# Kernel tuning notes

Measured on AMD Instinct MI355X. Metric: run time of the kernel, lower is better.

## Reference

```python
import jax, jax.numpy as jnp
import numpy as np

N_EMBD = 1024
N_HEAD = 16
HEAD = N_EMBD // N_HEAD  # 64
N_HIDDEN = 2816          # ((int(2*4*1024/3)-1)//256)*256 + 256
BLOCK_SIZE = 4096
EPS = 1e-5


def rope_cos_sin(T, hd, base=10000.0):
    theta = 1.0 / (base ** (jnp.arange(0, hd, 2, dtype=jnp.float32) / hd))  # (hd/2,)
    idx = jnp.arange(T, dtype=jnp.float32)
    ang = jnp.outer(idx, theta)  # (T, hd/2)
    return jnp.cos(ang), jnp.sin(ang)


def apply_rope(x, cos, sin):
    # x: (B, H, T, hd); rotate interleaved pairs (x0,x1),(x2,x3),...
    xp = x.reshape(*x.shape[:-1], HEAD // 2, 2)
    xe, xo = xp[..., 0], xp[..., 1]
    c = cos[None, None, :, :]
    s = sin[None, None, :, :]
    oe = xe * c - xo * s
    oo = xe * s + xo * c
    return jnp.stack([oe, oo], axis=-1).reshape(x.shape)


def rmsnorm(x, scale):
    ms = jnp.mean(x * x, axis=-1, keepdims=True)
    return scale * (x * jax.lax.rsqrt(ms + EPS))


def setup_inputs() -> dict:
    key = jax.random.key(0)
    ks = jax.random.split(key, 9)
    B, T = 2, 2048
    x = jax.random.normal(ks[0], (B, T, N_EMBD), dtype=jnp.float32)
    y_mask = jax.random.randint(ks[1], (B, 64), 0, 2, dtype=jnp.int32)
    sd = 1.0 / np.sqrt(N_EMBD)
    Wqkv = jax.random.normal(ks[2], (N_EMBD, 3 * N_EMBD), dtype=jnp.float32) * sd
    Wattn_proj = jax.random.normal(ks[3], (N_EMBD, N_EMBD), dtype=jnp.float32) * sd
    scale1 = jnp.ones((N_EMBD,), dtype=jnp.float32)
    scale2 = jnp.ones((N_EMBD,), dtype=jnp.float32)
    Wfc1 = jax.random.normal(ks[4], (N_EMBD, N_HIDDEN), dtype=jnp.float32) * sd
    Wfc2 = jax.random.normal(ks[5], (N_EMBD, N_HIDDEN), dtype=jnp.float32) * sd
    Wmlp_proj = jax.random.normal(ks[6], (N_HIDDEN, N_EMBD), dtype=jnp.float32) / np.sqrt(N_HIDDEN)
    return {"x": x, "y_mask": y_mask, "Wqkv": Wqkv, "Wattn_proj": Wattn_proj,
            "scale1": scale1, "scale2": scale2, "Wfc1": Wfc1, "Wfc2": Wfc2,
            "Wmlp_proj": Wmlp_proj}


def reference(x, y_mask, Wqkv, Wattn_proj, scale1, scale2, Wfc1, Wfc2, Wmlp_proj):
    B, T, C = x.shape
    # ---- attention branch (pre-RMSNorm) ----
    h = rmsnorm(x, scale1)
    qkv = h @ Wqkv  # (B, T, 3C)
    q, k, v = jnp.split(qkv, 3, axis=-1)
    q = q.reshape(B, T, N_HEAD, HEAD).transpose(0, 2, 1, 3)
    k = k.reshape(B, T, N_HEAD, HEAD).transpose(0, 2, 1, 3)
    v = v.reshape(B, T, N_HEAD, HEAD).transpose(0, 2, 1, 3)
    cos, sin = rope_cos_sin(T, HEAD)
    q = apply_rope(q, cos, sin)
    k = apply_rope(k, cos, sin)
    # mixed causal + text-text bidirectional mask
    causal = jnp.tril(jnp.ones((T, T), dtype=bool))  # (T, T)
    ym = y_mask.astype(bool)  # (B, L)
    L = ym.shape[1]
    text = ym[:, :, None] & ym[:, None, :]  # (B, L, L)
    text = jnp.pad(text, ((0, 0), (0, T - L), (0, T - L)))
    mask = jnp.logical_or(causal[None, :, :], text)  # (B, T, T)
    scale = 1.0 / np.sqrt(HEAD)
    scores = jnp.einsum('bhqd,bhkd->bhqk', q, k) * scale
    scores = jnp.where(mask[:, None, :, :], scores, -jnp.inf)
    attn = jax.nn.softmax(scores, axis=-1)
    y = jnp.einsum('bhqk,bhkd->bhqd', attn, v)
    y = y.transpose(0, 2, 1, 3).reshape(B, T, C)
    x = x + y @ Wattn_proj
    # ---- SwiGLU MLP branch (pre-RMSNorm) ----
    h2 = rmsnorm(x, scale2)
    m = jax.nn.silu(h2 @ Wfc1) * (h2 @ Wfc2)
    x = x + m @ Wmlp_proj
    return x
```

## Files before the change

### kernel.cpp

```cpp
#include <hip/hip_runtime.h>
#include <stdint.h>

typedef unsigned short u16;
typedef __attribute__((ext_vector_type(8))) short bf16x8;
typedef __attribute__((ext_vector_type(4))) float f32x4;

__device__ __forceinline__ float b2f(u16 u) {
    union { float f; uint32_t u; } v; v.u = ((uint32_t)u) << 16; return v.f;
}
__device__ __forceinline__ u16 f2b(float f) {
    union { float f; uint32_t u; } v; v.f = f;
    uint32_t r = v.u + 0x7FFFu + ((v.u >> 16) & 1u);
    return (u16)(r >> 16);
}

template <int CTRL>
__device__ __forceinline__ float dppf(float x) {
    union { float f; int i; } u; u.f = x;
    u.i = __builtin_amdgcn_update_dpp(0, u.i, CTRL, 0xF, 0xF, false);
    return u.f;
}
__device__ __forceinline__ float rowmax16(float v) {
    v = fmaxf(v, dppf<0x121>(v));
    v = fmaxf(v, dppf<0x122>(v));
    v = fmaxf(v, dppf<0x124>(v));
    v = fmaxf(v, dppf<0x128>(v));
    return v;
}
__device__ __forceinline__ float rowsum16(float v) {
    v += dppf<0x121>(v);
    v += dppf<0x122>(v);
    v += dppf<0x124>(v);
    v += dppf<0x128>(v);
    return v;
}

__device__ __forceinline__ void stage16(const void* g, void* l) {
    __builtin_amdgcn_global_load_lds(
        (const __attribute__((address_space(1))) uint32_t*)(uintptr_t)g,
        (__attribute__((address_space(3))) uint32_t*)(uint32_t)(uintptr_t)l,
        16, 0, 0);
}

__global__ __launch_bounds__(256) void transpose_all(const float* __restrict__ Wqkv,
                                                     const float* __restrict__ Wattn,
                                                     const float* __restrict__ Wfc1,
                                                     const float* __restrict__ Wfc2,
                                                     const float* __restrict__ Wmlp,
                                                     u16* WtQ, u16* WtA, u16* WtF1,
                                                     u16* WtF2, u16* WtM) {
    __shared__ u16 tile[32][33];
    int id = blockIdx.x;
    const float* src; u16* dst; int R, C;
    if (id < 3072)      {             src = Wqkv;  dst = WtQ;  R = 1024; C = 3072; }
    else if (id < 4096) { id -= 3072; src = Wattn; dst = WtA;  R = 1024; C = 1024; }
    else if (id < 6912) { id -= 4096; src = Wfc1;  dst = WtF1; R = 1024; C = 2816; }
    else if (id < 9728) { id -= 6912; src = Wfc2;  dst = WtF2; R = 1024; C = 2816; }
    else                { id -= 9728; src = Wmlp;  dst = WtM;  R = 2816; C = 1024; }
    const int nbx = C >> 5;
    const int bx = id % nbx, by = id / nbx;
    const int cx = bx * 32, ry = by * 32;
    const int tx = threadIdx.x, ty = threadIdx.y;
    #pragma unroll
    for (int i = 0; i < 32; i += 8)
        tile[ty + i][tx] = f2b(src[(size_t)(ry + ty + i) * C + cx + tx]);
    __syncthreads();
    #pragma unroll
    for (int i = 0; i < 32; i += 8)
        dst[(size_t)(cx + ty + i) * R + ry + tx] = tile[tx][ty + i];
}

__global__ __launch_bounds__(256) void rmsnorm_f32(const float* __restrict__ xin,
                                                   const float* __restrict__ scale,
                                                   u16* __restrict__ out) {
    const int row = blockIdx.x, tid = threadIdx.x;
    const float4 v = ((const float4*)(xin + (size_t)row * 1024))[tid];
    float ss = v.x * v.x + v.y * v.y + v.z * v.z + v.w * v.w;
    #pragma unroll
    for (int d = 32; d; d >>= 1) ss += __shfl_xor(ss, d);
    __shared__ float wsum[4];
    if ((tid & 63) == 0) wsum[tid >> 6] = ss;
    __syncthreads();
    const float r = rsqrtf((wsum[0] + wsum[1] + wsum[2] + wsum[3]) * (1.f / 1024.f) + 1e-5f);
    const float4 sc = ((const float4*)scale)[tid];
    uint2 o;
    o.x = (uint32_t)f2b(v.x * sc.x * r) | ((uint32_t)f2b(v.y * sc.y * r) << 16);
    o.y = (uint32_t)f2b(v.z * sc.z * r) | ((uint32_t)f2b(v.w * sc.w * r) << 16);
    ((uint2*)(out + (size_t)row * 1024))[tid] = o;
}

__global__ __launch_bounds__(256) void rope_kernel(u16* __restrict__ qkv) {
    const int gid = blockIdx.x * 256 + threadIdx.x;
    const int i = gid & 31;
    const int row = gid >> 5;
    const int tpos = row & 2047;
    const float theta = expf(-(float)i * (9.210340371976184f / 32.0f));
    const float ang = (float)tpos * theta;
    const float c = cosf(ang), s = sinf(ang);
    uint32_t* p = (uint32_t*)qkv + (size_t)row * 1536 + i;
    #pragma unroll
    for (int h = 0; h < 16; ++h) {
        const uint32_t uq = p[h * 32];
        {
            const float xe = b2f((u16)(uq & 0xffff)), xo = b2f((u16)(uq >> 16));
            p[h * 32] = (uint32_t)f2b(xe * c - xo * s) |
                        ((uint32_t)f2b(xe * s + xo * c) << 16);
        }
        const uint32_t uk = p[512 + h * 32];
        {
            const float xe = b2f((u16)(uk & 0xffff)), xo = b2f((u16)(uk >> 16));
            p[512 + h * 32] = (uint32_t)f2b(xe * c - xo * s) |
                              ((uint32_t)f2b(xe * s + xo * c) << 16);
        }
    }
}

template <int EPI>
__global__ __launch_bounds__(256) void gemm_bt(const u16* __restrict__ A,
                                               const u16* __restrict__ Bt,
                                               void* __restrict__ Cout,
                                               const void* __restrict__ Res,
                                               int N, int K) {
    __shared__ __attribute__((aligned(16))) u16 As[2][128 * 32];
    __shared__ __attribute__((aligned(16))) u16 Bs[2][128 * 32];
    const int tid = threadIdx.x;
    const int w = tid >> 6, lane = tid & 63;
    const int quad = lane >> 4, t = lane & 15;
    const int m0 = blockIdx.y * 128, n0 = blockIdx.x * 128;
    const int wm = (w >> 1) * 64, wn = (w & 1) * 64;

    const int srow = w * 16 + (lane >> 2);
    const int scol = (lane & 3) * 8;
    const u16* pA0 = A + (size_t)(m0 + srow) * K + scol;
    const u16* pA1 = pA0 + (size_t)64 * K;
    const u16* pB0 = Bt + (size_t)(n0 + srow) * K + scol;
    const u16* pB1 = pB0 + (size_t)64 * K;

    f32x4 acc[4][4];
    #pragma unroll
    for (int i = 0; i < 4; ++i)
        #pragma unroll
        for (int j = 0; j < 4; ++j) acc[i][j] = (f32x4){0.f, 0.f, 0.f, 0.f};

    for (int kb = 0; kb < K; kb += 64) {
        __syncthreads();
        stage16(pA0 + kb,      (char*)As[0] + w * 1024);
        stage16(pA1 + kb,      (char*)As[0] + 4096 + w * 1024);
        stage16(pB0 + kb,      (char*)Bs[0] + w * 1024);
        stage16(pB1 + kb,      (char*)Bs[0] + 4096 + w * 1024);
        stage16(pA0 + kb + 32, (char*)As[1] + w * 1024);
        stage16(pA1 + kb + 32, (char*)As[1] + 4096 + w * 1024);
        stage16(pB0 + kb + 32, (char*)Bs[1] + w * 1024);
        stage16(pB1 + kb + 32, (char*)Bs[1] + 4096 + w * 1024);
        __syncthreads();
        #pragma unroll
        for (int hf = 0; hf < 2; ++hf) {
            bf16x8 af[4], bfr[4];
            #pragma unroll
            for (int mi = 0; mi < 4; ++mi)
                af[mi] = *(const bf16x8*)((char*)As[hf] + (wm + mi * 16 + t) * 64 + quad * 16);
            #pragma unroll
            for (int ni = 0; ni < 4; ++ni)
                bfr[ni] = *(const bf16x8*)((char*)Bs[hf] + (wn + ni * 16 + t) * 64 + quad * 16);
            #pragma unroll
            for (int mi = 0; mi < 4; ++mi)
                #pragma unroll
                for (int ni = 0; ni < 4; ++ni)
                    acc[mi][ni] = __builtin_amdgcn_mfma_f32_16x16x32_bf16(af[mi], bfr[ni],
                                                                         acc[mi][ni], 0, 0, 0);
        }
    }
    #pragma unroll
    for (int mi = 0; mi < 4; ++mi) {
        const int row0 = m0 + wm + mi * 16 + quad * 4;
        #pragma unroll
        for (int ni = 0; ni < 4; ++ni) {
            const int col = n0 + wn + ni * 16 + t;
            #pragma unroll
            for (int r = 0; r < 4; ++r) {
                const size_t idx = (size_t)(row0 + r) * N + col;
                const float v = acc[mi][ni][r];
                if (EPI == 0) {
                    ((u16*)Cout)[idx] = f2b(v);
                } else if (EPI == 1) {
                    ((float*)Cout)[idx] = v + ((const float*)Res)[idx];
                } else {
                    const float av = b2f(((const u16*)Res)[idx]);
                    ((u16*)Cout)[idx] = f2b((av / (1.f + __expf(-av))) * v);
                }
            }
        }
    }
}

template <int EPI>
__global__ __launch_bounds__(256) void gemm_bt64(const u16* __restrict__ A,
                                                 const u16* __restrict__ Bt,
                                                 void* __restrict__ Cout,
                                                 const float* __restrict__ Res,
                                                 int N, int K) {
    __shared__ __attribute__((aligned(16))) u16 As[2][128 * 32];
    __shared__ __attribute__((aligned(16))) u16 Bs[2][64 * 32];
    const int tid = threadIdx.x;
    const int w = tid >> 6, lane = tid & 63;
    const int quad = lane >> 4, t = lane & 15;
    const int m0 = blockIdx.y * 128, n0 = blockIdx.x * 64;
    const int wm = (w >> 1) * 64, wn = (w & 1) * 32;

    const int srow = w * 16 + (lane >> 2);
    const int scol = (lane & 3) * 8;
    const u16* pA0 = A + (size_t)(m0 + srow) * K + scol;
    const u16* pA1 = pA0 + (size_t)64 * K;
    const u16* pB0 = Bt + (size_t)(n0 + srow) * K + scol;

    f32x4 acc[4][2];
    #pragma unroll
    for (int i = 0; i < 4; ++i)
        #pragma unroll
        for (int j = 0; j < 2; ++j) acc[i][j] = (f32x4){0.f, 0.f, 0.f, 0.f};

    for (int kb = 0; kb < K; kb += 64) {
        __syncthreads();
        stage16(pA0 + kb,      (char*)As[0] + w * 1024);
        stage16(pA1 + kb,      (char*)As[0] + 4096 + w * 1024);
        stage16(pB0 + kb,      (char*)Bs[0] + w * 1024);
        stage16(pA0 + kb + 32, (char*)As[1] + w * 1024);
        stage16(pA1 + kb + 32, (char*)As[1] + 4096 + w * 1024);
        stage16(pB0 + kb + 32, (char*)Bs[1] + w * 1024);
        __syncthreads();
        #pragma unroll
        for (int hf = 0; hf < 2; ++hf) {
            bf16x8 af[4], bfr[2];
            #pragma unroll
            for (int mi = 0; mi < 4; ++mi)
                af[mi] = *(const bf16x8*)((char*)As[hf] + (wm + mi * 16 + t) * 64 + quad * 16);
            #pragma unroll
            for (int ni = 0; ni < 2; ++ni)
                bfr[ni] = *(const bf16x8*)((char*)Bs[hf] + (wn + ni * 16 + t) * 64 + quad * 16);
            #pragma unroll
            for (int mi = 0; mi < 4; ++mi)
                #pragma unroll
                for (int ni = 0; ni < 2; ++ni)
                    acc[mi][ni] = __builtin_amdgcn_mfma_f32_16x16x32_bf16(af[mi], bfr[ni],
                                                                         acc[mi][ni], 0, 0, 0);
        }
    }
    #pragma unroll
    for (int mi = 0; mi < 4; ++mi) {
        const int row0 = m0 + wm + mi * 16 + quad * 4;
        #pragma unroll
        for (int ni = 0; ni < 2; ++ni) {
            const int col = n0 + wn + ni * 16 + t;
            #pragma unroll
            for (int r = 0; r < 4; ++r) {
                const size_t idx = (size_t)(row0 + r) * N + col;
                const float v = acc[mi][ni][r];
                if (EPI == 0) ((u16*)Cout)[idx]   = f2b(v);
                else          ((float*)Cout)[idx] = v + Res[idx];
            }
        }
    }
}

__global__ __launch_bounds__(256) void attn_kernel(const u16* __restrict__ qkv,
                                                   const int* __restrict__ ymask,
                                                   u16* __restrict__ y) {
    const int gid = blockIdx.x;
    const int xcd = gid & 7;
    const int j2 = gid >> 3;
    const int slot = j2 >> 4;
    const int pairk = j2 & 15;
    const int group = slot * 8 + xcd;
    const int h = group & 15, b = group >> 4;
    const int tid = threadIdx.x;
    const int w = tid >> 6, lane = tid & 63;
    const int quad = lane >> 4, t = lane & 15;

    __shared__ __attribute__((aligned(16))) u16 Ks[64 * 72];
    __shared__ __attribute__((aligned(16))) u16 Vts[64 * 72];
    __shared__ __attribute__((aligned(16))) u16 Ps[4][16 * 72];
    __shared__ int ymL[64];
    if (pairk == 0 && tid < 64) ymL[tid] = ymask[b * 64 + tid];

    const int skey = tid >> 3, sdg = tid & 7;
    const u16* pK = qkv + (size_t)(b * 2048 + skey) * 3072 + h * 64 + sdg * 8 + 1024;
    const int sblk0 = (skey >> 3) ^ sdg;
    const int sblk1 = (4 + (skey >> 3)) ^ sdg;

    for (int seg = 0; seg < 2; ++seg) {
        const int qt = seg ? pairk : 31 - pairk;
        const int q0 = qt * 64;

        bf16x8 aQ[2];
        {
            const u16* qp = qkv + (size_t)(b * 2048 + q0 + w * 16 + t) * 3072 + h * 64 + quad * 8;
            aQ[0] = *(const bf16x8*)qp;
            aQ[1] = *(const bf16x8*)(qp + 32);
            #pragma unroll
            for (int i = 0; i < 8; ++i) {
                aQ[0][i] = (short)f2b(b2f((u16)aQ[0][i]) * 0.125f);
                aQ[1][i] = (short)f2b(b2f((u16)aQ[1][i]) * 0.125f);
            }
        }

        f32x4 accO[4] = {(f32x4){0,0,0,0},(f32x4){0,0,0,0},(f32x4){0,0,0,0},(f32x4){0,0,0,0}};
        float mOld[4] = {-INFINITY, -INFINITY, -INFINITY, -INFINITY};
        float lSum[4] = {0.f, 0.f, 0.f, 0.f};

        for (int kb = 0; kb <= qt; ++kb) {
            const u16* pk = pK + (size_t)kb * 196608;
            const uint4 kv0 = *(const uint4*)pk;
            const uint4 vv0 = *(const uint4*)(pk + 1024);
            const uint4 kv1 = *(const uint4*)(pk + 98304);
            const uint4 vv1 = *(const uint4*)(pk + 99328);
            __syncthreads();
            *(uint4*)((char*)Ks + skey * 144 + sdg * 16) = kv0;
            *(uint4*)((char*)Ks + (skey + 32) * 144 + sdg * 16) = kv1;
            {
                const u16* vp0 = (const u16*)&vv0;
                const u16* vp1 = (const u16*)&vv1;
                #pragma unroll
                for (int jj = 0; jj < 8; ++jj) {
                    const int row = sdg * 8 + jj;
                    Vts[row * 72 + sblk0 * 8 + (skey & 7)] = vp0[jj];
                    Vts[row * 72 + sblk1 * 8 + (skey & 7)] = vp1[jj];
                }
            }
            __syncthreads();

            float s[4][4];
            __builtin_amdgcn_s_setprio(1);
            #pragma unroll
            for (int ni = 0; ni < 4; ++ni) {
                bf16x8 bK0 = *(const bf16x8*)((char*)Ks + (ni * 16 + t) * 144 + quad * 16);
                bf16x8 bK1 = *(const bf16x8*)((char*)Ks + (ni * 16 + t) * 144 + 64 + quad * 16);
                f32x4 sa = (f32x4){0.f, 0.f, 0.f, 0.f};
                sa = __builtin_amdgcn_mfma_f32_16x16x32_bf16(aQ[0], bK0, sa, 0, 0, 0);
                sa = __builtin_amdgcn_mfma_f32_16x16x32_bf16(aQ[1], bK1, sa, 0, 0, 0);
                #pragma unroll
                for (int r = 0; r < 4; ++r) s[ni][r] = sa[r];
            }
            __builtin_amdgcn_s_setprio(0);

            if (kb == qt) {
                const int irow = q0 + w * 16 + quad * 4;
                #pragma unroll
                for (int ni = 0; ni < 4; ++ni)
                    #pragma unroll
                    for (int r = 0; r < 4; ++r) {
                        const int i = irow + r, j = kb * 64 + ni * 16 + t;
                        const bool ok = (j <= i) || (qt == 0 && ymL[i & 63] && ymL[j & 63]);
                        if (!ok) s[ni][r] = -INFINITY;
                    }
            }

            float alpha[4];
            bool upd = false;
            #pragma unroll
            for (int r = 0; r < 4; ++r) {
                float mt = fmaxf(fmaxf(s[0][r], s[1][r]), fmaxf(s[2][r], s[3][r]));
                mt = rowmax16(mt);
                const float mNew = fmaxf(mOld[r], mt);
                upd = upd || (mNew > mOld[r]);
                alpha[r] = __expf(mOld[r] - mNew);
                #pragma unroll
                for (int ni = 0; ni < 4; ++ni) s[ni][r] = __expf(s[ni][r] - mNew);
                mOld[r] = mNew;
            }

            u16* Pw = Ps[w];
            #pragma unroll
            for (int ni = 0; ni < 4; ++ni)
                #pragma unroll
                for (int r = 0; r < 4; ++r)
                    Pw[(quad * 4 + r) * 72 + ni * 16 + t] = f2b(s[ni][r]);

            #pragma unroll
            for (int r = 0; r < 4; ++r) {
                float rs = (s[0][r] + s[1][r]) + (s[2][r] + s[3][r]);
                rs = rowsum16(rs);
                lSum[r] = lSum[r] * alpha[r] + rs;
            }
            if (__any(upd)) {
                #pragma unroll
                for (int dt = 0; dt < 4; ++dt)
                    #pragma unroll
                    for (int r = 0; r < 4; ++r) accO[dt][r] *= alpha[r];
            }

            bf16x8 aP0 = *(const bf16x8*)((char*)Pw + t * 144 + quad * 16);
            bf16x8 aP1 = *(const bf16x8*)((char*)Pw + t * 144 + 64 + quad * 16);
            __builtin_amdgcn_s_setprio(1);
            #pragma unroll
            for (int dt = 0; dt < 4; ++dt) {
                const int row = dt * 16 + t, rb = row >> 3;
                bf16x8 bV0 = *(const bf16x8*)((char*)Vts + row * 144 + ((quad ^ rb) << 4));
                bf16x8 bV1 = *(const bf16x8*)((char*)Vts + row * 144 + (((4 + quad) ^ rb) << 4));
                accO[dt] = __builtin_amdgcn_mfma_f32_16x16x32_bf16(aP0, bV0, accO[dt], 0, 0, 0);
                accO[dt] = __builtin_amdgcn_mfma_f32_16x16x32_bf16(aP1, bV1, accO[dt], 0, 0, 0);
            }
            __builtin_amdgcn_s_setprio(0);
        }
        const int orow = q0 + w * 16 + quad * 4;
        #pragma unroll
        for (int dt = 0; dt < 4; ++dt)
            #pragma unroll
            for (int r = 0; r < 4; ++r) {
                const size_t idx = (size_t)(b * 2048 + orow + r) * 1024 + h * 64 + dt * 16 + t;
                y[idx] = f2b(accO[dt][r] / lSum[r]);
            }
    }
}

extern "C" void kernel_launch(void* const* d_in, const int* in_sizes, int n_in,
                              void* d_out, int out_size, void* d_ws, size_t ws_size,
                              hipStream_t stream) {
    const float* x     = (const float*)d_in[0];
    const int*   ym    = (const int*)d_in[1];
    const float* Wqkv  = (const float*)d_in[2];
    const float* Wattn = (const float*)d_in[3];
    const float* s1    = (const float*)d_in[4];
    const float* s2    = (const float*)d_in[5];
    const float* Wfc1  = (const float*)d_in[6];
    const float* Wfc2  = (const float*)d_in[7];
    const float* Wmlp  = (const float*)d_in[8];

    char* ws = (char*)d_ws;
    u16*   h    = (u16*)(ws + 0);
    u16*   qkv  = (u16*)(ws + 8388608);
    u16*   fc1  = qkv;
    float* xr   = (float*)(ws + 33554432);
    u16*   WtA  = (u16*)(ws + 50331648);
    u16*   WtF1 = (u16*)(ws + 52428800);
    u16*   WtF2 = (u16*)(ws + 58195968);
    u16*   WtM  = (u16*)(ws + 63963136);
    u16*   WtQ  = (u16*)(ws + 73400320);
    const dim3 tb(32, 8);

    transpose_all<<<12544, tb, 0, stream>>>(Wqkv, Wattn, Wfc1, Wfc2, Wmlp,
                                            WtQ, WtA, WtF1, WtF2, WtM);
    rmsnorm_f32<<<4096, 256, 0, stream>>>(x, s1, h);
    gemm_bt<0><<<dim3(24, 32), 256, 0, stream>>>(h, WtQ, qkv, nullptr, 3072, 1024);
    rope_kernel<<<512, 256, 0, stream>>>(qkv);
    attn_kernel<<<512, 256, 0, stream>>>(qkv, ym, h);
    gemm_bt64<1><<<dim3(16, 32), 256, 0, stream>>>(h, WtA, xr, x, 1024, 1024);
    rmsnorm_f32<<<4096, 256, 0, stream>>>(xr, s2, h);
    gemm_bt<0><<<dim3(22, 32), 256, 0, stream>>>(h, WtF1, fc1, nullptr, 2816, 1024);
    gemm_bt<2><<<dim3(22, 32), 256, 0, stream>>>(h, WtF2, fc1, fc1, 2816, 1024);
    gemm_bt64<1><<<dim3(16, 32), 256, 0, stream>>>(fc1, WtM, (float*)d_out, xr, 1024, 2816);
}
```

Baseline: 370.1 us.

## Fuse SwiGLU fc1 and fc2 GEMMs into one dual-accumulator kernel

Replaces two separate GEMMs (fc1 writing bf16, then fc2 reading fc1 back for the SiLU-multiply epilogue) with one kernel. It loads the A tile once and accumulates both products in two register accumulators, applying silu(a)*b at store time. This removes the bf16 round-trip of the fc1 intermediate and one reload of the A operand. In exchange the tile shrinks to 128x64 with doubled accumulators per wave, which raises register pressure and could lower occupancy.

Result: faster. 351.8 us (-4.9%).

```diff
diff --git a/kernel.cpp b/kernel.cpp
--- a/kernel.cpp
+++ b/kernel.cpp
@@ -180,14 +180,8 @@
             for (int r = 0; r < 4; ++r) {
                 const size_t idx = (size_t)(row0 + r) * N + col;
                 const float v = acc[mi][ni][r];
-                if (EPI == 0) {
-                    ((u16*)Cout)[idx] = f2b(v);
-                } else if (EPI == 1) {
-                    ((float*)Cout)[idx] = v + ((const float*)Res)[idx];
-                } else {
-                    const float av = b2f(((const u16*)Res)[idx]);
-                    ((u16*)Cout)[idx] = f2b((av / (1.f + __expf(-av))) * v);
-                }
+                if (EPI == 0) ((u16*)Cout)[idx]   = f2b(v);
+                else          ((float*)Cout)[idx] = v + ((const float*)Res)[idx];
             }
         }
     }
@@ -262,6 +256,85 @@
     }
 }
 
+__global__ __launch_bounds__(256) void gemm_fc(const u16* __restrict__ A,
+                                               const u16* __restrict__ B1t,
+                                               const u16* __restrict__ B2t,
+                                               u16* __restrict__ Cout,
+                                               int N, int K) {
+    __shared__ __attribute__((aligned(16))) u16 As[2][128 * 32];
+    __shared__ __attribute__((aligned(16))) u16 B1s[2][64 * 32];
+    __shared__ __attribute__((aligned(16))) u16 B2s[2][64 * 32];
+    const int tid = threadIdx.x;
+    const int w = tid >> 6, lane = tid & 63;
+    const int quad = lane >> 4, t = lane & 15;
+    const int m0 = blockIdx.y * 128, n0 = blockIdx.x * 64;
+    const int wm = (w >> 1) * 64, wn = (w & 1) * 32;
+
+    const int srow = w * 16 + (lane >> 2);
+    const int scol = (lane & 3) * 8;
+    const u16* pA0 = A + (size_t)(m0 + srow) * K + scol;
+    const u16* pA1 = pA0 + (size_t)64 * K;
+    const u16* pB1 = B1t + (size_t)(n0 + srow) * K + scol;
+    const u16* pB2 = B2t + (size_t)(n0 + srow) * K + scol;
+
+    f32x4 acc1[4][2], acc2[4][2];
+    #pragma unroll
+    for (int i = 0; i < 4; ++i)
+        #pragma unroll
+        for (int j = 0; j < 2; ++j) {
+            acc1[i][j] = (f32x4){0.f, 0.f, 0.f, 0.f};
+            acc2[i][j] = (f32x4){0.f, 0.f, 0.f, 0.f};
+        }
+
+    for (int kb = 0; kb < K; kb += 64) {
+        __syncthreads();
+        stage16(pA0 + kb,      (char*)As[0] + w * 1024);
+        stage16(pA1 + kb,      (char*)As[0] + 4096 + w * 1024);
+        stage16(pB1 + kb,      (char*)B1s[0] + w * 1024);
+        stage16(pB2 + kb,      (char*)B2s[0] + w * 1024);
+        stage16(pA0 + kb + 32, (char*)As[1] + w * 1024);
+        stage16(pA1 + kb + 32, (char*)As[1] + 4096 + w * 1024);
+        stage16(pB1 + kb + 32, (char*)B1s[1] + w * 1024);
+        stage16(pB2 + kb + 32, (char*)B2s[1] + w * 1024);
+        __syncthreads();
+        #pragma unroll
+        for (int hf = 0; hf < 2; ++hf) {
+            bf16x8 af[4], b1r[2], b2r[2];
+            #pragma unroll
+            for (int mi = 0; mi < 4; ++mi)
+                af[mi] = *(const bf16x8*)((char*)As[hf] + (wm + mi * 16 + t) * 64 + quad * 16);
+            #pragma unroll
+            for (int ni = 0; ni < 2; ++ni) {
+                b1r[ni] = *(const bf16x8*)((char*)B1s[hf] + (wn + ni * 16 + t) * 64 + quad * 16);
+                b2r[ni] = *(const bf16x8*)((char*)B2s[hf] + (wn + ni * 16 + t) * 64 + quad * 16);
+            }
+            #pragma unroll
+            for (int mi = 0; mi < 4; ++mi)
+                #pragma unroll
+                for (int ni = 0; ni < 2; ++ni) {
+                    acc1[mi][ni] = __builtin_amdgcn_mfma_f32_16x16x32_bf16(af[mi], b1r[ni],
+                                                                          acc1[mi][ni], 0, 0, 0);
+                    acc2[mi][ni] = __builtin_amdgcn_mfma_f32_16x16x32_bf16(af[mi], b2r[ni],
+                                                                          acc2[mi][ni], 0, 0, 0);
+                }
+        }
+    }
+    #pragma unroll
+    for (int mi = 0; mi < 4; ++mi) {
+        const int row0 = m0 + wm + mi * 16 + quad * 4;
+        #pragma unroll
+        for (int ni = 0; ni < 2; ++ni) {
+            const int col = n0 + wn + ni * 16 + t;
+            #pragma unroll
+            for (int r = 0; r < 4; ++r) {
+                const size_t idx = (size_t)(row0 + r) * N + col;
+                const float a = acc1[mi][ni][r];
+                Cout[idx] = f2b((a / (1.f + __expf(-a))) * acc2[mi][ni][r]);
+            }
+        }
+    }
+}
+
 __global__ __launch_bounds__(256) void attn_kernel(const u16* __restrict__ qkv,
                                                    const int* __restrict__ ymask,
                                                    u16* __restrict__ y) {
@@ -445,7 +518,6 @@
     attn_kernel<<<512, 256, 0, stream>>>(qkv, ym, h);
     gemm_bt64<1><<<dim3(16, 32), 256, 0, stream>>>(h, WtA, xr, x, 1024, 1024);
     rmsnorm_f32<<<4096, 256, 0, stream>>>(xr, s2, h);
-    gemm_bt<0><<<dim3(22, 32), 256, 0, stream>>>(h, WtF1, fc1, nullptr, 2816, 1024);
-    gemm_bt<2><<<dim3(22, 32), 256, 0, stream>>>(h, WtF2, fc1, fc1, 2816, 1024);
+    gemm_fc<<<dim3(44, 32), 256, 0, stream>>>(h, WtF1, WtF2, fc1, 2816, 1024);
     gemm_bt64<1><<<dim3(16, 32), 256, 0, stream>>>(fc1, WtM, (float*)d_out, xr, 1024, 2816);
 }
```
